# Performance work log

Hardware: AMD Instinct MI355X
Metric: run time of the kernel (lower is better)

## Reference

```python
import jax, jax.numpy as jnp
import numpy as np

N, D = 16384, 256


def setup_inputs() -> dict:
    key = jax.random.key(0)
    k1, k2 = jax.random.split(key)
    # L2-normalized CLIP-style embeddings
    img = jax.random.normal(k1, (N, D), dtype=jnp.float32)
    txt = jax.random.normal(k2, (N, D), dtype=jnp.float32)
    img = img / jnp.linalg.norm(img, axis=-1, keepdims=True)
    txt = txt / jnp.linalg.norm(txt, axis=-1, keepdims=True)
    return {
        "image_features": img,
        "text_features": txt,
        "logit_scale": jnp.float32(np.log(10.0)),  # SigLIP init t' = log 10
        "logit_bias": jnp.float32(-10.0),          # SigLIP init b = -10
        "curvature": jnp.float32(1.0),             # unused for geometry='clip'
    }


def reference(image_features, text_features, logit_scale, logit_bias, curvature):
    n = image_features.shape[0]
    # logits = scale * (x @ y.T) + bias   (cosine_similarity metric)
    logits = logit_scale * jnp.einsum("nd,md->nm", image_features, text_features) + logit_bias
    # labels = 2*I - 1: +1 on diagonal, -1 off-diagonal. Instead of materializing
    # labels, flip logit sign off-diagonal via where on the identity pattern.
    eye = jnp.eye(n, dtype=bool)
    signed = jnp.where(eye, logits, -logits)  # labels * logits
    loss = -jnp.sum(jax.nn.log_sigmoid(signed)) / n
    return loss
```

## Files before the change

kernel.cpp:

```cpp
#include <hip/hip_runtime.h>
#include <hip/hip_bf16.h>
#include <hip/hip_fp8.h>

#define NROWS 16384
#define DDIM  256
#define LOG2E 1.44269504088896f

typedef __attribute__((ext_vector_type(8))) int ix8;
typedef __attribute__((ext_vector_type(4))) short bh4;
typedef __attribute__((ext_vector_type(4))) float fx4;
typedef __attribute__((ext_vector_type(16))) float fx16;

__device__ __forceinline__ short f2bf(float x) {
  __hip_bfloat16 h = __float2bfloat16(x);
  return *reinterpret_cast<short*>(&h);
}

__device__ __forceinline__ float fexp2(float x) {
#if __has_builtin(__builtin_amdgcn_exp2f)
  return __builtin_amdgcn_exp2f(x);
#else
  return __expf(x * 0.6931471805599453f);
#endif
}

__device__ __forceinline__ fx16 fzero16() {
  fx16 z;
#pragma unroll
  for (int q = 0; q < 16; ++q) z[q] = 0.f;
  return z;
}

__device__ __forceinline__ float softplus_f(float y) {
  float a = fabsf(y);
  float t = __expf(-a);
  float l;
  if (t < 0.125f) {
    l = t * (1.0f - t * (0.5f - 0.333333333f * t));
  } else {
    l = log1pf(t);
  }
  return fmaxf(y, 0.0f) + l;
}

__global__ void cast_fp8_kernel(const float* __restrict__ in,
                                unsigned char* __restrict__ out) {
  int i = (blockIdx.x * blockDim.x + threadIdx.x) * 8;
  float4 v0 = *(const float4*)(in + i);
  float4 v1 = *(const float4*)(in + i + 4);
  unsigned r0 = (unsigned)__hip_fp8_e4m3(v0.x).__x |
                ((unsigned)__hip_fp8_e4m3(v0.y).__x << 8) |
                ((unsigned)__hip_fp8_e4m3(v0.z).__x << 16) |
                ((unsigned)__hip_fp8_e4m3(v0.w).__x << 24);
  unsigned r1 = (unsigned)__hip_fp8_e4m3(v1.x).__x |
                ((unsigned)__hip_fp8_e4m3(v1.y).__x << 8) |
                ((unsigned)__hip_fp8_e4m3(v1.z).__x << 16) |
                ((unsigned)__hip_fp8_e4m3(v1.w).__x << 24);
  uint2 r; r.x = r0; r.y = r1;
  *(uint2*)(out + i) = r;
}


#define MFMA_SC(A_, B_, C_)                                                    \
  __builtin_amdgcn_mfma_scale_f32_32x32x64_f8f6f4((A_), (B_), (C_), 0, 0, 0,  \
                                                  sc1, 0, sc1)

#define STAGE(bt2, kc2, bufp)                                                  \
  do {                                                                         \
    _Pragma("unroll")                                                          \
    for (int it_ = 0; it_ < 2; ++it_) {                                        \
      __builtin_amdgcn_global_load_lds(                                        \
          (const __attribute__((address_space(1))) void*)(                     \
              Bm +                                                             \
              (size_t)(colgbase + (bt2) * 128 + it_ * 64 + (wave & 1) * 32 +   \
                       (lane >> 1)) * 256 +                                    \
              (kc2) * 64 + (wave >> 1) * 32 + (lane & 1) * 16),                \
          (__attribute__((address_space(3))) void*)((bufp) + it_ * 4096 +      \
                                                    wave * 1024 + lane * 16),  \
          16, 0, 0);                                                           \
    }                                                                          \
  } while (0)

#define CHUNKF(kc, rbuf, VM, DO_ST, SBT, SKC, sq)                              \
  do {                                                                         \
    asm volatile("s_waitcnt vmcnt(%0)" ::"i"(VM) : "memory");                  \
    __builtin_amdgcn_s_barrier();                                              \
    asm volatile("" ::: "memory");         \
    ix8 b0_ = *(const ix8*)((rbuf) + bb);                                      \
    ix8 b1_ = *(const ix8*)((rbuf) + 1024 + bb);                               \
    if (DO_ST) STAGE(SBT, SKC, sq);                                            \
    acc00 = MFMA_SC(areg[0][kc], b0_, acc00);                                  \
    acc01 = MFMA_SC(areg[0][kc], b1_, acc01);                                  \
    acc10 = MFMA_SC(areg[1][kc], b0_, acc10);                                  \
    acc11 = MFMA_SC(areg[1][kc], b1_, acc11);                                  \
  } while (0)

#define EPI32(A_, m_, n_)                                                      \
  do {                                                                         \
    fx16 v_ = A_;                                                              \
    A_ = fzero16();                                                            \
    _Pragma("unroll")                                                          \
    for (int g_ = 0; g_ < 16; g_ += 4) {                                       \
      e0 += fexp2(k1 * v_[g_ + 0]);                                            \
      e1 += fexp2(k1 * v_[g_ + 1]);                                            \
      e2 += fexp2(k1 * v_[g_ + 2]);                                            \
      e3 += fexp2(k1 * v_[g_ + 3]);                                            \
    }                                                                          \
    if (dtile) {                     \
      const int gcol_ = colbase + wc * 64 + (n_) * 32 + (lane & 31);           \
      const int grow0_ = rowbase + wr * 64 + (m_) * 32 + 4 * hi;               \
      _Pragma("unroll")                                                        \
      for (int r_ = 0; r_ < 16; ++r_) {                                        \
        int grow_ = grow0_ + (r_ & 3) + 8 * (r_ >> 2);                         \
        if (grow_ == gcol_) {                                                  \
          d += softplus_f(-fmaf(scale, v_[r_], bias));                         \
          e0 -= fexp2(k1 * v_[r_]);                                            \
        }                                                                      \
      }                                                                        \
    }                                                                          \
  } while (0)

#define EPILOGUE(btv)                                                          \
  do {                                                                         \
    const int colbase = colgbase + (btv) * 128;                                \
    const bool dtile = (colbase == rowbase);                                   \
    EPI32(acc00, 0, 0); EPI32(acc01, 0, 1);                                    \
    EPI32(acc10, 1, 0); EPI32(acc11, 1, 1);                                    \
  } while (0)

__global__ __launch_bounds__(256, 2) void siglip_strip(
    const unsigned char* __restrict__ Am, const unsigned char* __restrict__ Bm,
    const float* __restrict__ scale_p, const float* __restrict__ bias_p,
    float* __restrict__ out) {
  __shared__ char lds[32768];
  char* q0 = lds;
  char* q1 = lds + 8192;
  char* q2 = lds + 16384;
  char* q3 = lds + 24576;

  const int tid  = threadIdx.x;
  const int lane = tid & 63;
  const int wave = tid >> 6;
  const int wr   = wave >> 1;
  const int wc   = wave & 1;
  const int bid  = blockIdx.x;
  const int rp   = ((bid >> 3) << 1) | (bid & 1);
  const int cg   = (bid >> 1) & 3;
  const int rowbase  = rp * 128;
  const int colgbase = cg * 4096;

  const int hi  = lane >> 5;
  const int bb  = wc * 4096 + hi * 2048 + (lane & 31) * 32;
  const int sc1 = 0x7F7F7F7F;

  const float scale = *scale_p;
  const float bias  = *bias_p;
  const float k1 = scale * LOG2E;
  const float eb = fexp2(bias * LOG2E);

  ix8 areg[2][4];
  {
    const unsigned char* Aw = Am + (size_t)(rowbase + wr * 64) * 256;
#pragma unroll
    for (int m = 0; m < 2; ++m)
#pragma unroll
      for (int kc = 0; kc < 4; ++kc)
        areg[m][kc] = *(const ix8*)(Aw + (size_t)(m * 32 + (lane & 31)) * 256 +
                                    kc * 64 + hi * 32);
  }
  asm volatile("s_waitcnt vmcnt(0)" ::: "memory");

  STAGE(0, 0, q0);
  STAGE(0, 1, q1);
  STAGE(0, 2, q2);

  fx16 acc00 = fzero16(), acc01 = fzero16();
  fx16 acc10 = fzero16(), acc11 = fzero16();
  float e0 = 0.f, e1 = 0.f, e2 = 0.f, e3 = 0.f, d = 0.f;

  for (int bt = 0; bt < 31; ++bt) {
    CHUNKF(0, q0, 4, 1, bt,     3, q3);
    CHUNKF(1, q1, 4, 1, bt + 1, 0, q0);
    CHUNKF(2, q2, 4, 1, bt + 1, 1, q1);
    CHUNKF(3, q3, 4, 1, bt + 1, 2, q2);
    EPILOGUE(bt);
  }
  CHUNKF(0, q0, 4, 1, 31, 3, q3);
  CHUNKF(1, q1, 4, 0, 0, 0, q0);
  CHUNKF(2, q2, 2, 0, 0, 0, q0);
  CHUNKF(3, q3, 0, 0, 0, 0, q0);
  EPILOGUE(31);

  float local = fmaf((e0 + e1) + (e2 + e3), eb, d);
#pragma unroll
  for (int off = 32; off > 0; off >>= 1) local += __shfl_xor(local, off, 64);

  __syncthreads();
  float* red = (float*)lds;
  if (lane == 0) red[wave] = local;
  __syncthreads();
  if (tid == 0)
    atomicAdd(out, ((red[0] + red[1]) + (red[2] + red[3])) * (1.0f / 16384.0f));
}

__device__ __forceinline__ unsigned swz256(unsigned o) {
  return o ^ (((o >> 8) & 7u) << 4);
}

__device__ __forceinline__ void map_tile(int bid, int& tr, int& tc) {
  int xcd = bid & 7;
  int idx = bid >> 3;
  int g   = idx >> 7;
  int w   = idx & 127;
  tr = xcd * 16 + (w >> 3);
  tc = g * 8 + (w & 7);
}

typedef __attribute__((ext_vector_type(8))) short bh8;

__global__ __launch_bounds__(256, 2) void siglip_fallback(
    const float* __restrict__ A, const float* __restrict__ B,
    const float* __restrict__ scale_p, const float* __restrict__ bias_p,
    float* __restrict__ out) {
  __shared__ char lds[65536];
  char* ldsA = lds;
  char* ldsB = lds + 32768;
  const int tid  = threadIdx.x;
  const int lane = tid & 63;
  const int wave = tid >> 6;
  const int wr   = wave >> 1;
  const int wc   = wave & 1;
  int tr, tc;
  map_tile(blockIdx.x, tr, tc);
  const int brow = tr * 128, bcol = tc * 128;

  fx4 acc[4][4];
#pragma unroll
  for (int m = 0; m < 4; ++m)
#pragma unroll
    for (int n = 0; n < 4; ++n) acc[m][n] = (fx4){0.f, 0.f, 0.f, 0.f};

#pragma unroll
  for (int p = 0; p < 2; ++p) {
    __syncthreads();
    const float* Af = A + (size_t)brow * DDIM + p * 128;
    const float* Bf = B + (size_t)bcol * DDIM + p * 128;
#pragma unroll
    for (int it = 0; it < 16; ++it) {
      int c = it * 256 + tid;
      int row = c >> 5, j = c & 31;
      unsigned o = row * 256 + j * 8;
      {
        float4 v = *(const float4*)(Af + (size_t)row * DDIM + j * 4);
        bh4 h;
        h[0] = f2bf(v.x); h[1] = f2bf(v.y); h[2] = f2bf(v.z); h[3] = f2bf(v.w);
        *(bh4*)(ldsA + swz256(o)) = h;
      }
      {
        float4 v = *(const float4*)(Bf + (size_t)row * DDIM + j * 4);
        bh4 h;
        h[0] = f2bf(v.x); h[1] = f2bf(v.y); h[2] = f2bf(v.z); h[3] = f2bf(v.w);
        *(bh4*)(ldsB + swz256(o)) = h;
      }
    }
    __syncthreads();
#pragma unroll
    for (int kk = 0; kk < 4; ++kk) {
      const int colb = kk * 64 + (lane >> 4) * 16;
      bh8 a[4], b[4];
#pragma unroll
      for (int m = 0; m < 4; ++m) {
        int r = wr * 64 + m * 16 + (lane & 15);
        a[m] = *(const bh8*)(ldsA + swz256((unsigned)(r * 256 + colb)));
      }
#pragma unroll
      for (int n = 0; n < 4; ++n) {
        int r = wc * 64 + n * 16 + (lane & 15);
        b[n] = *(const bh8*)(ldsB + swz256((unsigned)(r * 256 + colb)));
      }
#pragma unroll
      for (int m = 0; m < 4; ++m)
#pragma unroll
        for (int n = 0; n < 4; ++n)
          acc[m][n] = __builtin_amdgcn_mfma_f32_16x16x32_bf16(a[m], b[n],
                                                              acc[m][n], 0, 0, 0);
    }
  }

  const float scale = *scale_p;
  const float bias  = *bias_p;
  const float k1 = scale * LOG2E;
  const float k0 = bias * LOG2E;
  float s0 = 0.f, s1 = 0.f, s2 = 0.f, s3 = 0.f;
  const int  row0 = brow + wr * 64 + (lane >> 4) * 4;
  const int  col0 = bcol + wc * 64 + (lane & 15);
  const bool isdiag = (tr == tc);
#pragma unroll
  for (int m = 0; m < 4; ++m) {
#pragma unroll
    for (int n = 0; n < 4; ++n) {
      fx4 v = acc[m][n];
      s0 += fexp2(fmaf(k1, v[0], k0));
      s1 += fexp2(fmaf(k1, v[1], k0));
      s2 += fexp2(fmaf(k1, v[2], k0));
      s3 += fexp2(fmaf(k1, v[3], k0));
      if (isdiag) {
        const int gj = col0 + n * 16;
#pragma unroll
        for (int j = 0; j < 4; ++j) {
          const int gi = row0 + m * 16 + j;
          if (gi == gj) {
            float logit = fmaf(scale, v[j], bias);
            s0 += softplus_f(-logit) - fexp2(fmaf(k1, v[j], k0));
          }
        }
      }
    }
  }
  float local = (s0 + s1) + (s2 + s3);
#pragma unroll
  for (int off = 32; off > 0; off >>= 1) local += __shfl_xor(local, off, 64);

  __syncthreads();
  float* red = (float*)lds;
  if (lane == 0) red[wave] = local;
  __syncthreads();
  if (tid == 0)
    atomicAdd(out, (red[0] + red[1] + red[2] + red[3]) * (1.0f / 16384.0f));
}

extern "C" void kernel_launch(void* const* d_in, const int* in_sizes, int n_in,
                              void* d_out, int out_size, void* d_ws,
                              size_t ws_size, hipStream_t stream) {
  const float* img     = (const float*)d_in[0];
  const float* txt     = (const float*)d_in[1];
  const float* scale_p = (const float*)d_in[2];
  const float* bias_p  = (const float*)d_in[3];
  float* out = (float*)d_out;

  hipMemsetAsync(d_out, 0, (size_t)out_size * sizeof(float), stream);

  const size_t elems = (size_t)NROWS * DDIM;
  const size_t need  = 2 * elems * sizeof(unsigned char);

  if (ws_size >= need) {
    unsigned char* A8 = (unsigned char*)d_ws;
    unsigned char* B8 = A8 + elems;
    const int cast_blocks = (int)(elems / (256 * 8));
    cast_fp8_kernel<<<cast_blocks, 256, 0, stream>>>(img, A8);
    cast_fp8_kernel<<<cast_blocks, 256, 0, stream>>>(txt, B8);
    siglip_strip<<<512, 256, 0, stream>>>(A8, B8, scale_p, bias_p, out);
    return;
  }
  const int nblocks = (NROWS / 128) * (NROWS / 128);
  siglip_fallback<<<nblocks, 256, 0, stream>>>(img, txt, scale_p, bias_p, out);
}
```

Before: 98.60 us.

## Software-pipeline LDS fragment reads one chunk ahead of MFMAs

Restructures the K-chunk loop so each step reads the next chunk's B fragments from LDS into ping-pong registers while running MFMAs on fragments loaded in the previous step. A fourth stage buffer is prefetched up front, so all four LDS buffers are in flight. The aim is to hide LDS read latency behind matrix ops. In exchange it uses more VGPRs, which may lower occupancy, and it adds an lgkmcnt wait before each barrier.

```diff
diff --git a/kernel.cpp b/kernel.cpp
--- a/kernel.cpp
+++ b/kernel.cpp
@@ -81,18 +81,29 @@
     }                                                                          \
   } while (0)
 
-#define CHUNKF(kc, rbuf, VM, DO_ST, SBT, SKC, sq)                              \
-  do {                                                                         \
+#define READF(P, qbuf)                                                         \
+  do {                                                                         \
+    P##0 = *(const ix8*)((qbuf) + bb);                                         \
+    P##1 = *(const ix8*)((qbuf) + 1024 + bb);                                  \
+  } while (0)
+
+#define MFMAS(kc, P)                                                           \
+  do {                                                                         \
+    acc00 = MFMA_SC(areg[0][kc], P##0, acc00);                                 \
+    acc01 = MFMA_SC(areg[0][kc], P##1, acc01);                                 \
+    acc10 = MFMA_SC(areg[1][kc], P##0, acc10);                                 \
+    acc11 = MFMA_SC(areg[1][kc], P##1, acc11);                                 \
+  } while (0)
+
+#define CHUNKP(kc, CUR, NXT, qn, VM, DO_RD, DO_ST, SBT, SKC, sq)               \
+  do {                                                                         \
+    asm volatile("s_waitcnt lgkmcnt(0)" ::: "memory");                         \
     asm volatile("s_waitcnt vmcnt(%0)" ::"i"(VM) : "memory");                  \
     __builtin_amdgcn_s_barrier();                                              \
     asm volatile("" ::: "memory");         \
-    ix8 b0_ = *(const ix8*)((rbuf) + bb);                                      \
-    ix8 b1_ = *(const ix8*)((rbuf) + 1024 + bb);                               \
+    if (DO_RD) READF(NXT, qn);                                                 \
     if (DO_ST) STAGE(SBT, SKC, sq);                                            \
-    acc00 = MFMA_SC(areg[0][kc], b0_, acc00);                                  \
-    acc01 = MFMA_SC(areg[0][kc], b1_, acc01);                                  \
-    acc10 = MFMA_SC(areg[1][kc], b0_, acc10);                                  \
-    acc11 = MFMA_SC(areg[1][kc], b1_, acc11);                                  \
+    MFMAS(kc, CUR);                                                            \
   } while (0)
 
 #define EPI32(A_, m_, n_)                                                      \
@@ -173,22 +184,30 @@
   STAGE(0, 0, q0);
   STAGE(0, 1, q1);
   STAGE(0, 2, q2);
+  STAGE(0, 3, q3);
 
   fx16 acc00 = fzero16(), acc01 = fzero16();
   fx16 acc10 = fzero16(), acc11 = fzero16();
   float e0 = 0.f, e1 = 0.f, e2 = 0.f, e3 = 0.f, d = 0.f;
 
+  ix8 fe0, fe1, fo0, fo1;
+
+  asm volatile("s_waitcnt vmcnt(6)" ::: "memory");
+  __builtin_amdgcn_s_barrier();
+  asm volatile("" ::: "memory");
+  READF(fe, q0);
+
   for (int bt = 0; bt < 31; ++bt) {
-    CHUNKF(0, q0, 4, 1, bt,     3, q3);
-    CHUNKF(1, q1, 4, 1, bt + 1, 0, q0);
-    CHUNKF(2, q2, 4, 1, bt + 1, 1, q1);
-    CHUNKF(3, q3, 4, 1, bt + 1, 2, q2);
+    CHUNKP(0, fe, fo, q1, 4, 1, 1, bt + 1, 0, q0);
+    CHUNKP(1, fo, fe, q2, 4, 1, 1, bt + 1, 1, q1);
+    CHUNKP(2, fe, fo, q3, 4, 1, 1, bt + 1, 2, q2);
+    CHUNKP(3, fo, fe, q0, 4, 1, 1, bt + 1, 3, q3);
     EPILOGUE(bt);
   }
-  CHUNKF(0, q0, 4, 1, 31, 3, q3);
-  CHUNKF(1, q1, 4, 0, 0, 0, q0);
-  CHUNKF(2, q2, 2, 0, 0, 0, q0);
-  CHUNKF(3, q3, 0, 0, 0, 0, q0);
+  CHUNKP(0, fe, fo, q1, 4, 1, 0, 0, 0, q0);
+  CHUNKP(1, fo, fe, q2, 2, 1, 0, 0, 0, q0);
+  CHUNKP(2, fe, fo, q3, 0, 1, 0, 0, 0, q0);
+  MFMAS(3, fo);
   EPILOGUE(31);
 
   float local = fmaf((e0 + e1) + (e2 + e3), eb, d);
```

New measurement: 96.30 us. 1.02x faster.

## Fold logit scale into fp8 image cast and double grid with shorter column strips

Applied to the files above, without the earlier changes.

Multiplies the image features by scale*log2(e) during the fp8 cast, so the MFMA output is already in exp2 units and the epilogue drops one multiply per element. The grid grows from 512 to 1024 blocks, each covering a 2048-column strip instead of 4096, with a simpler block-to-tile mapping and launch bounds raised to request 4 blocks per SIMD. This aims for more parallelism and a cheaper epilogue, at the cost of more per-block prologue work (A register loads, pipeline fill) and extra fp8 quantization error from the scaled values.

```diff
diff --git a/kernel.cpp b/kernel.cpp
--- a/kernel.cpp
+++ b/kernel.cpp
@@ -5,6 +5,7 @@
 #define NROWS 16384
 #define DDIM  256
 #define LOG2E 1.44269504088896f
+#define LN2   0.69314718055995f
 
 typedef __attribute__((ext_vector_type(8))) int ix8;
 typedef __attribute__((ext_vector_type(4))) short bh4;
@@ -44,18 +45,21 @@
 }
 
 __global__ void cast_fp8_kernel(const float* __restrict__ in,
-                                unsigned char* __restrict__ out) {
+                                unsigned char* __restrict__ out,
+                                const float* __restrict__ scale_p,
+                                int do_scale) {
+  const float s = do_scale ? (*scale_p * LOG2E) : 1.0f;
   int i = (blockIdx.x * blockDim.x + threadIdx.x) * 8;
   float4 v0 = *(const float4*)(in + i);
   float4 v1 = *(const float4*)(in + i + 4);
-  unsigned r0 = (unsigned)__hip_fp8_e4m3(v0.x).__x |
-                ((unsigned)__hip_fp8_e4m3(v0.y).__x << 8) |
-                ((unsigned)__hip_fp8_e4m3(v0.z).__x << 16) |
-                ((unsigned)__hip_fp8_e4m3(v0.w).__x << 24);
-  unsigned r1 = (unsigned)__hip_fp8_e4m3(v1.x).__x |
-                ((unsigned)__hip_fp8_e4m3(v1.y).__x << 8) |
-                ((unsigned)__hip_fp8_e4m3(v1.z).__x << 16) |
-                ((unsigned)__hip_fp8_e4m3(v1.w).__x << 24);
+  unsigned r0 = (unsigned)__hip_fp8_e4m3(v0.x * s).__x |
+                ((unsigned)__hip_fp8_e4m3(v0.y * s).__x << 8) |
+                ((unsigned)__hip_fp8_e4m3(v0.z * s).__x << 16) |
+                ((unsigned)__hip_fp8_e4m3(v0.w * s).__x << 24);
+  unsigned r1 = (unsigned)__hip_fp8_e4m3(v1.x * s).__x |
+                ((unsigned)__hip_fp8_e4m3(v1.y * s).__x << 8) |
+                ((unsigned)__hip_fp8_e4m3(v1.z * s).__x << 16) |
+                ((unsigned)__hip_fp8_e4m3(v1.w * s).__x << 24);
   uint2 r; r.x = r0; r.y = r1;
   *(uint2*)(out + i) = r;
 }
@@ -101,10 +105,10 @@
     A_ = fzero16();                                                            \
     _Pragma("unroll")                                                          \
     for (int g_ = 0; g_ < 16; g_ += 4) {                                       \
-      e0 += fexp2(k1 * v_[g_ + 0]);                                            \
-      e1 += fexp2(k1 * v_[g_ + 1]);                                            \
-      e2 += fexp2(k1 * v_[g_ + 2]);                                            \
-      e3 += fexp2(k1 * v_[g_ + 3]);                                            \
+      e0 += fexp2(v_[g_ + 0]);                                                 \
+      e1 += fexp2(v_[g_ + 1]);                                                 \
+      e2 += fexp2(v_[g_ + 2]);                                                 \
+      e3 += fexp2(v_[g_ + 3]);                                                 \
     }                                                                          \
     if (dtile) {                     \
       const int gcol_ = colbase + wc * 64 + (n_) * 32 + (lane & 31);           \
@@ -113,8 +117,8 @@
       for (int r_ = 0; r_ < 16; ++r_) {                                        \
         int grow_ = grow0_ + (r_ & 3) + 8 * (r_ >> 2);                         \
         if (grow_ == gcol_) {                                                  \
-          d += softplus_f(-fmaf(scale, v_[r_], bias));                         \
-          e0 -= fexp2(k1 * v_[r_]);                                            \
+          d += softplus_f(-fmaf(v_[r_], LN2, bias));      \
+          e0 -= fexp2(v_[r_]);                                                 \
         }                                                                      \
       }                                                                        \
     }                                                                          \
@@ -128,7 +132,7 @@
     EPI32(acc10, 1, 0); EPI32(acc11, 1, 1);                                    \
   } while (0)
 
-__global__ __launch_bounds__(256, 2) void siglip_strip(
+__global__ __launch_bounds__(256, 4) void siglip_strip(
     const unsigned char* __restrict__ Am, const unsigned char* __restrict__ Bm,
     const float* __restrict__ scale_p, const float* __restrict__ bias_p,
     float* __restrict__ out) {
@@ -144,19 +148,17 @@
   const int wr   = wave >> 1;
   const int wc   = wave & 1;
   const int bid  = blockIdx.x;
-  const int rp   = ((bid >> 3) << 1) | (bid & 1);
-  const int cg   = (bid >> 1) & 3;
+  const int cg   = bid & 7;
+  const int rp   = bid >> 3;
   const int rowbase  = rp * 128;
-  const int colgbase = cg * 4096;
+  const int colgbase = cg * 2048;
 
   const int hi  = lane >> 5;
   const int bb  = wc * 4096 + hi * 2048 + (lane & 31) * 32;
   const int sc1 = 0x7F7F7F7F;
 
-  const float scale = *scale_p;
-  const float bias  = *bias_p;
-  const float k1 = scale * LOG2E;
-  const float eb = fexp2(bias * LOG2E);
+  const float bias = *bias_p;
+  const float eb = fexp2((*scale_p) * 0.0f + bias * LOG2E);
 
   ix8 areg[2][4];
   {
@@ -178,18 +180,18 @@
   fx16 acc10 = fzero16(), acc11 = fzero16();
   float e0 = 0.f, e1 = 0.f, e2 = 0.f, e3 = 0.f, d = 0.f;
 
-  for (int bt = 0; bt < 31; ++bt) {
+  for (int bt = 0; bt < 15; ++bt) {
     CHUNKF(0, q0, 4, 1, bt,     3, q3);
     CHUNKF(1, q1, 4, 1, bt + 1, 0, q0);
     CHUNKF(2, q2, 4, 1, bt + 1, 1, q1);
     CHUNKF(3, q3, 4, 1, bt + 1, 2, q2);
     EPILOGUE(bt);
   }
-  CHUNKF(0, q0, 4, 1, 31, 3, q3);
+  CHUNKF(0, q0, 4, 1, 15, 3, q3);
   CHUNKF(1, q1, 4, 0, 0, 0, q0);
   CHUNKF(2, q2, 2, 0, 0, 0, q0);
   CHUNKF(3, q3, 0, 0, 0, 0, q0);
-  EPILOGUE(31);
+  EPILOGUE(15);
 
   float local = fmaf((e0 + e1) + (e2 + e3), eb, d);
 #pragma unroll
@@ -347,9 +349,9 @@
     unsigned char* A8 = (unsigned char*)d_ws;
     unsigned char* B8 = A8 + elems;
     const int cast_blocks = (int)(elems / (256 * 8));
-    cast_fp8_kernel<<<cast_blocks, 256, 0, stream>>>(img, A8);
-    cast_fp8_kernel<<<cast_blocks, 256, 0, stream>>>(txt, B8);
-    siglip_strip<<<512, 256, 0, stream>>>(A8, B8, scale_p, bias_p, out);
+    cast_fp8_kernel<<<cast_blocks, 256, 0, stream>>>(img, A8, scale_p, 1);
+    cast_fp8_kernel<<<cast_blocks, 256, 0, stream>>>(txt, B8, scale_p, 0);
+    siglip_strip<<<1024, 256, 0, stream>>>(A8, B8, scale_p, bias_p, out);
     return;
   }
   const int nblocks = (NROWS / 128) * (NROWS / 128);
```

Measured after the change: 303.3 us. 3.08x slower.
